# Kernel optimization log

Hardware: AMD Instinct MI355X
Metric: run time of the kernel (lower is better)

## Reference

```python
import jax, jax.numpy as jnp
import numpy as np

NUM_HEAD = 16
D_MODEL = 1024


def setup_inputs() -> dict:
    key = jax.random.key(0)
    ks = jax.random.split(key, 11)
    B, S, D = 2, 2048, D_MODEL
    scale = 1.0 / np.sqrt(D)
    inp = {
        "q": jax.random.normal(ks[0], (B, S, D), dtype=jnp.float32),
        "k": jax.random.normal(ks[1], (B, S, D), dtype=jnp.float32),
        "v": jax.random.normal(ks[2], (B, S, D), dtype=jnp.float32),
        "Wq": jax.random.normal(ks[3], (D, D), dtype=jnp.float32) * scale,
        "bq": jnp.zeros((D,), dtype=jnp.float32),
        "Wk": jax.random.normal(ks[4], (D, D), dtype=jnp.float32) * scale,
        "bk": jnp.zeros((D,), dtype=jnp.float32),
        "Wv": jax.random.normal(ks[5], (D, D), dtype=jnp.float32) * scale,
        "bv": jnp.zeros((D,), dtype=jnp.float32),
        "Wo": jax.random.normal(ks[6], (D, D), dtype=jnp.float32) * scale,
        "bo": jnp.zeros((D,), dtype=jnp.float32),
    }
    return inp


def _split_heads(x, num_head):
    B, S, D = x.shape
    return x.reshape(B, S, num_head, D // num_head).transpose(0, 2, 1, 3)  # [B,H,S,d]


def reference(q, k, v, Wq, bq, Wk, bk, Wv, bv, Wo, bo):
    H = NUM_HEAD
    qp = q @ Wq + bq
    kp = k @ Wk + bk  # computed but UNUSED, matching source bug
    vp = v @ Wv + bv
    # source bug: k := split_heads(v-projection)
    qh = _split_heads(qp, H)          # [B,H,S,d]
    kh = _split_heads(vp, H)          # [B,H,S,d]  (v-projection used as keys)
    vh = _split_heads(vp, H)          # [B,H,S,d]
    d = qh.shape[-1]
    scores = jnp.einsum('bhqd,bhkd->bhqk', qh, kh) / jnp.sqrt(jnp.asarray(d, qh.dtype))
    attn = jax.nn.softmax(scores, axis=-1)
    out = jnp.einsum('bhqk,bhkd->bhqd', attn, vh)  # [B,H,S,d]
    B, _, S, _ = out.shape
    out = out.transpose(0, 2, 1, 3).reshape(B, S, H * d)
    return out @ Wo + bo
```

## Files before the change

kernel.cpp:

```cpp
#include <hip/hip_runtime.h>
#include <hip/hip_bf16.h>

using bfrag  = __attribute__((ext_vector_type(8))) __bf16;
using f32x4  = __attribute__((ext_vector_type(4))) float;
using f32x16 = __attribute__((ext_vector_type(16))) float;
using v4u    = __attribute__((ext_vector_type(4))) unsigned int;
using v2u    = __attribute__((ext_vector_type(2))) unsigned int;

__device__ __forceinline__ ushort f2bf(float f) {
    union { float f; unsigned u; } c; c.f = f;
    return (ushort)((c.u + 0x7fffu + ((c.u >> 16) & 1u)) >> 16);
}

__device__ __forceinline__ float bf2f(ushort u) {
    union { unsigned u; float f; } c; c.u = (unsigned)u << 16; return c.f;
}

__device__ __forceinline__ unsigned pack_bf16x2(float lo, float hi) {
    union { __hip_bfloat162 h; unsigned u; } c;
    c.h = __float22bfloat162_rn(make_float2(lo, hi));
    return c.u;
}

__device__ __forceinline__ void gld_lds16(const ushort* g, ushort* l) {
    __builtin_amdgcn_global_load_lds(
        (const __attribute__((address_space(1))) void*)g,
        (__attribute__((address_space(3))) void*)l, 16, 0, 0);
}

__device__ __forceinline__ f32x16 mfma32(bfrag a, bfrag b, f32x16 c) {
    return __builtin_amdgcn_mfma_f32_32x32x16_bf16(a, b, c, 0, 0, 0);
}


__global__ void cvt_all(const float* __restrict__ s0, ushort* __restrict__ d0,
                        const float* __restrict__ s1, ushort* __restrict__ d1,
                        const float* __restrict__ s2, ushort* __restrict__ d2,
                        const float* __restrict__ q, ushort* __restrict__ qbf,
                        const float* __restrict__ v, ushort* __restrict__ vbf) {
    const int z = blockIdx.z;
    if (z < 3) {
        __shared__ float t[32][33];
        const float* src = z == 0 ? s0 : z == 1 ? s1 : s2;
        ushort* dst = z == 0 ? d0 : z == 1 ? d1 : d2;
        const int tx = threadIdx.x, ty = threadIdx.y;
        const int c0 = blockIdx.x * 32, r0 = blockIdx.y * 32;
        for (int i = ty; i < 32; i += 8) t[i][tx] = src[(size_t)(r0 + i) * 1024 + c0 + tx];
        __syncthreads();
        for (int i = ty; i < 32; i += 8) dst[(size_t)(c0 + i) * 1024 + r0 + tx] = f2bf(t[tx][i]);
    } else {
        const int tid = threadIdx.y * 32 + threadIdx.x;
        int i = ((z - 3) * 1024 + blockIdx.y * 32 + blockIdx.x) * 256 + tid;
        const float* s; ushort* d;
        if (i < 1048576) { s = q; d = qbf; } else { s = v; d = vbf; i -= 1048576; }
        float4 f = ((const float4*)s)[i];
        ((ushort4*)d)[i] = make_ushort4(f2bf(f.x), f2bf(f.y), f2bf(f.z), f2bf(f.w));
    }
}


__global__ __launch_bounds__(256) void vpt_T(const ushort* __restrict__ VPb, ushort* __restrict__ VPT) {
    __shared__ ushort T[64][72];
    const int st = blockIdx.x, bh = blockIdx.y;
    const int b = bh >> 4, h = bh & 15;
    const int tid = threadIdx.x;
#pragma unroll
    for (int i = 0; i < 2; ++i) {
        const int c = tid + i * 256;
        const int row = c >> 3, col8 = (c & 7) * 8;
        v4u d = *(const v4u*)(VPb + (size_t)(b * 2048 + st * 64 + row) * 1024 + h * 64 + col8);
        *(v4u*)&T[row][col8] = d;
    }
    __syncthreads();
    const int d = tid >> 2, sch = tid & 3;
    union { ushort s[16]; v4u v[2]; } tmp;
#pragma unroll
    for (int j = 0; j < 16; ++j) {
        const int js = (j & 3) | ((j >> 1) & 4) | ((j << 1) & 8);
        tmp.s[j] = T[sch * 16 + js][d];
    }
    ushort* dst = VPT + ((size_t)bh * 64 + d) * 2048 + st * 64 + sch * 16;
    *(v4u*)dst = tmp.v[0];
    *(v4u*)(dst + 8) = tmp.v[1];
}


template<bool BF16OUT>
__device__ __forceinline__ void gemm_body(
    const ushort* __restrict__ A, const ushort* __restrict__ Bt,
    const float* __restrict__ bias, void* __restrict__ Cout,
    float scale, int bM, int bN)
{
    __shared__ ushort As[2][64 * 32];
    __shared__ ushort Bs[2][128 * 32];
    const int tid = threadIdx.x;
    const int lane = tid & 63, w = tid >> 6;
    const int l15 = lane & 15, lg = lane >> 4;
    const int wr = w >> 1, wc = w & 1;

    const ushort* Ag = A + (size_t)bM * 64 * 1024;
    const ushort* Bg = Bt + (size_t)bN * 128 * 1024;
    const int ar = tid >> 2;
    const int cc = (tid & 3) * 8;

    auto STAGE = [&](int buf, int kt) {
        const int kk = kt * 32;
        gld_lds16(Ag + (size_t)ar * 1024 + kk + cc, &As[buf][tid * 8]);
#pragma unroll
        for (int i = 0; i < 2; ++i)
            gld_lds16(Bg + (size_t)(ar + i * 64) * 1024 + kk + cc, &Bs[buf][(tid + i * 256) * 8]);
    };

    f32x4 acc[2][4];
#pragma unroll
    for (int m = 0; m < 2; ++m)
#pragma unroll
        for (int n = 0; n < 4; ++n) acc[m][n] = (f32x4){0.f, 0.f, 0.f, 0.f};

    STAGE(0, 0);
    __syncthreads();
    int cur = 0;
    for (int kt = 0; kt < 32; ++kt) {
        if (kt < 31) STAGE(cur ^ 1, kt + 1);
        bfrag aF[2], bF[4];
#pragma unroll
        for (int m = 0; m < 2; ++m) aF[m] = *(const bfrag*)&As[cur][(wr * 32 + m * 16 + l15) * 32 + lg * 8];
#pragma unroll
        for (int n = 0; n < 4; ++n) bF[n] = *(const bfrag*)&Bs[cur][(wc * 64 + n * 16 + l15) * 32 + lg * 8];
        __builtin_amdgcn_s_setprio(1);
#pragma unroll
        for (int m = 0; m < 2; ++m)
#pragma unroll
            for (int n = 0; n < 4; ++n)
                acc[m][n] = __builtin_amdgcn_mfma_f32_16x16x32_bf16(aF[m], bF[n], acc[m][n], 0, 0, 0);
        __builtin_amdgcn_s_setprio(0);
        if (kt < 31) {
            __syncthreads();
            cur ^= 1;
        }
    }

#pragma unroll
    for (int m = 0; m < 2; ++m)
#pragma unroll
        for (int n = 0; n < 4; ++n) {
            const int gcol = bN * 128 + wc * 64 + n * 16 + l15;
            const float bv = bias[gcol];
#pragma unroll
            for (int j = 0; j < 4; ++j) {
                const int grow = bM * 64 + wr * 32 + m * 16 + lg * 4 + j;
                const float val = (acc[m][n][j] + bv) * scale;
                if constexpr (BF16OUT) {
                    ((ushort*)Cout)[(size_t)grow * 1024 + gcol] = f2bf(val);
                } else {
                    ((float*)Cout)[(size_t)grow * 1024 + gcol] = val;
                }
            }
        }
}

__global__ __launch_bounds__(256, 4) void gemm_qv(
    const ushort* __restrict__ Aq, const ushort* __restrict__ Wq, const float* __restrict__ bq, ushort* __restrict__ Cq,
    const ushort* __restrict__ Av, const ushort* __restrict__ Wv, const float* __restrict__ bv, ushort* __restrict__ Cv,
    float qscale)
{
    const int z = blockIdx.z;
    gemm_body<true>(z ? Av : Aq, z ? Wv : Wq, z ? bv : bq, z ? (void*)Cv : (void*)Cq,
                    z ? 1.0f : qscale, blockIdx.y, blockIdx.x);
}

__global__ __launch_bounds__(256, 4) void gemm_o(
    const ushort* __restrict__ A, const ushort* __restrict__ Bt,
    const float* __restrict__ bias, float* __restrict__ Cout)
{
    gemm_body<false>(A, Bt, bias, Cout, 1.0f, blockIdx.y, blockIdx.x);
}


__global__ __launch_bounds__(256, 2) void attn_kernel(
    const ushort* __restrict__ QP, const ushort* __restrict__ VP,
    const ushort* __restrict__ VPT, ushort* __restrict__ Opart, float* __restrict__ Lpart)
{
    __shared__ ushort Ks[2][4096];
    __shared__ ushort Vs[2][4096];
    const int tid = threadIdx.x;
    const int w = tid >> 6, lane = tid & 63;
    const int l31 = lane & 31, hi = lane >> 5;
    const int bh = blockIdx.x, qt = blockIdx.y, half = blockIdx.z;
    const int b = bh >> 4, h = bh & 15;
    const int qrow0 = qt * 256 + w * 64;
    const int k0 = half * 16;

    const int sr = lane >> 3;
    const int sc = ((lane & 7) ^ sr) * 8;
    const ushort* Kg = VP + (size_t)(b * 2048) * 1024 + h * 64 + sc;
    const ushort* Vg = VPT + (size_t)bh * 131072 + sc;

    auto STAGE = [&](int slot, int kt) {
#pragma unroll
        for (int i = 0; i < 2; ++i) {
            const int kb = w * 2 + i;
            const int r = kb * 8 + sr;
            gld_lds16(Kg + (size_t)(kt * 64 + r) * 1024, &Ks[slot][kb * 512]);
            gld_lds16(Vg + (size_t)r * 2048 + kt * 64, &Vs[slot][kb * 512]);
        }
    };

    const ushort* Qp = QP + ((size_t)(b * 2048 + qrow0 + l31)) * 1024 + h * 64 + hi * 8;
    bfrag qA[4], qBt[4];
#pragma unroll
    for (int ds = 0; ds < 4; ++ds) {
        qA[ds]  = *(const bfrag*)(Qp + ds * 16);
        qBt[ds] = *(const bfrag*)(Qp + 32 * 1024 + ds * 16);
    }

    f32x16 OA0, OA1, OB0, OB1;
#pragma unroll
    for (int r = 0; r < 16; ++r) { OA0[r] = 0.f; OA1[r] = 0.f; OB0[r] = 0.f; OB1[r] = 0.f; }
    float lrunA = 0.f, lrunB = 0.f;

    const int swz = (l31 & 7) << 4;
    const int cA = hi * 16;

    STAGE(0, k0);
    __syncthreads();

    auto SOFTMAX = [&](f32x16& S0, f32x16& S1, bfrag (&pB)[4], float& lrun) {
        float p[32];
#pragma unroll
        for (int r = 0; r < 16; ++r) {
            p[r]      = __builtin_amdgcn_exp2f(S0[r]);
            p[16 + r] = __builtin_amdgcn_exp2f(S1[r]);
        }
        float s8[8];
#pragma unroll
        for (int i = 0; i < 8; ++i) s8[i] = (p[i] + p[i + 8]) + (p[i + 16] + p[i + 24]);
        lrun += ((s8[0] + s8[1]) + (s8[2] + s8[3])) + ((s8[4] + s8[5]) + (s8[6] + s8[7]));
#pragma unroll
        for (int c = 0; c < 4; ++c) {
            union { v4u u; bfrag f; } cv;
#pragma unroll
            for (int wd = 0; wd < 4; ++wd)
                cv.u[wd] = pack_bf16x2(p[8 * c + 2 * wd], p[8 * c + 2 * wd + 1]);
            pB[c] = cv.f;
        }
    };

#pragma unroll 1
    for (int t = 0; t < 16; ++t) {
        if (t > 0) __syncthreads();
        if (t + 1 < 16) STAGE((t + 1) & 1, k0 + t + 1);
        const ushort* Kb_ = Ks[t & 1];
        const ushort* Vb_ = Vs[t & 1];

        bfrag k0f[4], k1f[4];
#pragma unroll
        for (int ds = 0; ds < 4; ++ds) {
            k0f[ds] = *(const bfrag*)&Kb_[(l31 * 128 + ((ds * 32 + cA) ^ swz)) >> 1];
            k1f[ds] = *(const bfrag*)&Kb_[((l31 + 32) * 128 + ((ds * 32 + cA) ^ swz)) >> 1];
        }
        f32x16 SA0, SA1, SB0, SB1;
#pragma unroll
        for (int r = 0; r < 16; ++r) { SA0[r] = -16.f; SA1[r] = -16.f; SB0[r] = -16.f; SB1[r] = -16.f; }
        __builtin_amdgcn_s_setprio(1);
#pragma unroll
        for (int ds = 0; ds < 4; ++ds) {
            SA0 = mfma32(k0f[ds], qA[ds], SA0);
            SA1 = mfma32(k1f[ds], qA[ds], SA1);
            SB0 = mfma32(k0f[ds], qBt[ds], SB0);
            SB1 = mfma32(k1f[ds], qBt[ds], SB1);
        }
        __builtin_amdgcn_s_setprio(0);

        bfrag pBA[4], pBB[4];
        SOFTMAX(SA0, SA1, pBA, lrunA);
        SOFTMAX(SB0, SB1, pBB, lrunB);

        bfrag vF0[4], vF1[4];
#pragma unroll
        for (int c = 0; c < 4; ++c) {
            vF0[c] = *(const bfrag*)&Vb_[(l31 * 128 + ((c * 32 + cA) ^ swz)) >> 1];
            vF1[c] = *(const bfrag*)&Vb_[((l31 + 32) * 128 + ((c * 32 + cA) ^ swz)) >> 1];
        }
        __builtin_amdgcn_s_setprio(1);
#pragma unroll
        for (int c = 0; c < 4; ++c) {
            OA0 = mfma32(vF0[c], pBA[c], OA0);
            OA1 = mfma32(vF1[c], pBA[c], OA1);
            OB0 = mfma32(vF0[c], pBB[c], OB0);
            OB1 = mfma32(vF1[c], pBB[c], OB1);
        }
        __builtin_amdgcn_s_setprio(0);
    }

    lrunA += __shfl_xor(lrunA, 32);
    lrunB += __shfl_xor(lrunB, 32);
    ushort* AoA = Opart + (size_t)half * 4194304
                + (size_t)(b * 2048 + qrow0 + l31) * 1024 + h * 64 + hi * 4;
    ushort* AoB = AoA + 32 * 1024;
#pragma unroll
    for (int t = 0; t < 2; ++t) {
#pragma unroll
        for (int g = 0; g < 4; ++g) {
            const float a0 = t ? OA1[4 * g + 0] : OA0[4 * g + 0];
            const float a1 = t ? OA1[4 * g + 1] : OA0[4 * g + 1];
            const float a2 = t ? OA1[4 * g + 2] : OA0[4 * g + 2];
            const float a3 = t ? OA1[4 * g + 3] : OA0[4 * g + 3];
            *(v2u*)(AoA + t * 32 + g * 8) = (v2u){pack_bf16x2(a0, a1), pack_bf16x2(a2, a3)};
            const float b0 = t ? OB1[4 * g + 0] : OB0[4 * g + 0];
            const float b1 = t ? OB1[4 * g + 1] : OB0[4 * g + 1];
            const float b2 = t ? OB1[4 * g + 2] : OB0[4 * g + 2];
            const float b3 = t ? OB1[4 * g + 3] : OB0[4 * g + 3];
            *(v2u*)(AoB + t * 32 + g * 8) = (v2u){pack_bf16x2(b0, b1), pack_bf16x2(b2, b3)};
        }
    }
    if (hi == 0) {
        Lpart[half * 65536 + bh * 2048 + qrow0 + l31] = lrunA;
        Lpart[half * 65536 + bh * 2048 + qrow0 + 32 + l31] = lrunB;
    }
}


__global__ __launch_bounds__(256) void combine_kernel(
    const ushort* __restrict__ Opart, const float* __restrict__ Lpart,
    ushort* __restrict__ AO)
{
    const int t = blockIdx.x * 256 + threadIdx.x;
    const int e0 = t * 8;
    const int grow = e0 >> 10, col = e0 & 1023;
    const int b = grow >> 11, s = grow & 2047, h = col >> 6;
    const int li = (b * 16 + h) * 2048 + s;
    const float l = Lpart[li] + Lpart[65536 + li];
    const float inv = 1.0f / l;
    v4u a = *(const v4u*)(Opart + e0);
    v4u c = *(const v4u*)(Opart + 4194304 + e0);
    v4u o;
#pragma unroll
    for (int wd = 0; wd < 4; ++wd) {
        const float x0 = (bf2f((ushort)(a[wd] & 0xffff)) + bf2f((ushort)(c[wd] & 0xffff))) * inv;
        const float x1 = (bf2f((ushort)(a[wd] >> 16))    + bf2f((ushort)(c[wd] >> 16)))    * inv;
        o[wd] = pack_bf16x2(x0, x1);
    }
    *(v4u*)(AO + e0) = o;
}


extern "C" void kernel_launch(void* const* d_in, const int* in_sizes, int n_in,
                              void* d_out, int out_size, void* d_ws, size_t ws_size,
                              hipStream_t stream) {
    (void)in_sizes; (void)n_in; (void)out_size; (void)ws_size;
    const float* q  = (const float*)d_in[0];
    const float* v  = (const float*)d_in[2];
    const float* Wq = (const float*)d_in[3];
    const float* bq = (const float*)d_in[4];
    const float* Wv = (const float*)d_in[7];
    const float* bv = (const float*)d_in[8];
    const float* Wo = (const float*)d_in[9];
    const float* bo = (const float*)d_in[10];
    float* out = (float*)d_out;
    char* ws = (char*)d_ws;
    const size_t MB = 1ull << 20;
    ushort* qbf = (ushort*)(ws + 0);
    ushort* vbf = (ushort*)(ws + 8 * MB);
    ushort* WqT = (ushort*)(ws + 16 * MB);
    ushort* WvT = (ushort*)(ws + 18 * MB);
    ushort* WoT = (ushort*)(ws + 20 * MB);
    ushort* QPb = (ushort*)(ws + 22 * MB);
    ushort* VPb = (ushort*)(ws + 30 * MB);
    ushort* VPT = (ushort*)(ws + 38 * MB);

    ushort* Opart = (ushort*)(ws + 0);
    float*  Lpart = (float*)(ws + 16 * MB);
    ushort* AO    = QPb;

    cvt_all<<<dim3(32, 32, 11), dim3(32, 8), 0, stream>>>(
        Wq, WqT, Wv, WvT, Wo, WoT, q, qbf, v, vbf);

    const float qscale = 0.125f * 1.44269504088896340736f;
    gemm_qv<<<dim3(8, 64, 2), 256, 0, stream>>>(qbf, WqT, bq, QPb,
                                                vbf, WvT, bv, VPb, qscale);
    vpt_T<<<dim3(32, 32), 256, 0, stream>>>(VPb, VPT);
    attn_kernel<<<dim3(32, 8, 2), 256, 0, stream>>>(QPb, VPb, VPT, Opart, Lpart);
    combine_kernel<<<2048, 256, 0, stream>>>(Opart, Lpart, AO);
    gemm_o<<<dim3(8, 64), 256, 0, stream>>>(AO, WoT, bo, out);
}
```

Baseline: 125.8 us.

## Fuse V transpose into QV GEMM epilogue and split-combine into output GEMM

The QV projection GEMM now stages its bf16 output tile in shared memory and writes the transposed V layout directly, so the separate vpt_T kernel is removed. The output projection GEMM now loads both split-K attention partials and the softmax denominators, combines and normalises them in registers, and writes the A tile to LDS itself, so the combine kernel and its intermediate buffer round trip are removed. This drops two launches and roughly 24MB of global traffic. In exchange, the A operand of gemm_o uses register-staged loads instead of direct-to-LDS copies, and both GEMMs have occupancy hints lowered from 4 to 3.

```diff
diff --git a/kernel.cpp b/kernel.cpp
--- a/kernel.cpp
+++ b/kernel.cpp
@@ -59,44 +59,24 @@
 }
 
 
-__global__ __launch_bounds__(256) void vpt_T(const ushort* __restrict__ VPb, ushort* __restrict__ VPT) {
-    __shared__ ushort T[64][72];
-    const int st = blockIdx.x, bh = blockIdx.y;
-    const int b = bh >> 4, h = bh & 15;
-    const int tid = threadIdx.x;
-#pragma unroll
-    for (int i = 0; i < 2; ++i) {
-        const int c = tid + i * 256;
-        const int row = c >> 3, col8 = (c & 7) * 8;
-        v4u d = *(const v4u*)(VPb + (size_t)(b * 2048 + st * 64 + row) * 1024 + h * 64 + col8);
-        *(v4u*)&T[row][col8] = d;
-    }
-    __syncthreads();
-    const int d = tid >> 2, sch = tid & 3;
-    union { ushort s[16]; v4u v[2]; } tmp;
-#pragma unroll
-    for (int j = 0; j < 16; ++j) {
-        const int js = (j & 3) | ((j >> 1) & 4) | ((j << 1) & 8);
-        tmp.s[j] = T[sch * 16 + js][d];
-    }
-    ushort* dst = VPT + ((size_t)bh * 64 + d) * 2048 + st * 64 + sch * 16;
-    *(v4u*)dst = tmp.v[0];
-    *(v4u*)(dst + 8) = tmp.v[1];
-}
-
-
-template<bool BF16OUT>
-__device__ __forceinline__ void gemm_body(
-    const ushort* __restrict__ A, const ushort* __restrict__ Bt,
-    const float* __restrict__ bias, void* __restrict__ Cout,
-    float scale, int bM, int bN)
+__global__ __launch_bounds__(256, 3) void gemm_qv(
+    const ushort* __restrict__ Aq, const ushort* __restrict__ Wq, const float* __restrict__ bq, ushort* __restrict__ Cq,
+    const ushort* __restrict__ Av, const ushort* __restrict__ Wv, const float* __restrict__ bv, ushort* __restrict__ Cv,
+    ushort* __restrict__ VPT, float qscale)
 {
-    __shared__ ushort As[2][64 * 32];
-    __shared__ ushort Bs[2][128 * 32];
+    __shared__ ushort SM[12288];
+    const int z = blockIdx.z;
+    const ushort* A  = z ? Av : Aq;
+    const ushort* Bt = z ? Wv : Wq;
+    const float* bias = z ? bv : bq;
+    ushort* Cout = z ? Cv : Cq;
+    const float scale = z ? 1.0f : qscale;
+
     const int tid = threadIdx.x;
     const int lane = tid & 63, w = tid >> 6;
     const int l15 = lane & 15, lg = lane >> 4;
     const int wr = w >> 1, wc = w & 1;
+    const int bM = blockIdx.y, bN = blockIdx.x;
 
     const ushort* Ag = A + (size_t)bM * 64 * 1024;
     const ushort* Bg = Bt + (size_t)bN * 128 * 1024;
@@ -105,10 +85,11 @@
 
     auto STAGE = [&](int buf, int kt) {
         const int kk = kt * 32;
-        gld_lds16(Ag + (size_t)ar * 1024 + kk + cc, &As[buf][tid * 8]);
+        gld_lds16(Ag + (size_t)ar * 1024 + kk + cc, &SM[buf * 2048 + tid * 8]);
 #pragma unroll
         for (int i = 0; i < 2; ++i)
-            gld_lds16(Bg + (size_t)(ar + i * 64) * 1024 + kk + cc, &Bs[buf][(tid + i * 256) * 8]);
+            gld_lds16(Bg + (size_t)(ar + i * 64) * 1024 + kk + cc,
+                      &SM[4096 + buf * 4096 + (tid + i * 256) * 8]);
     };
 
     f32x4 acc[2][4];
@@ -124,9 +105,11 @@
         if (kt < 31) STAGE(cur ^ 1, kt + 1);
         bfrag aF[2], bF[4];
 #pragma unroll
-        for (int m = 0; m < 2; ++m) aF[m] = *(const bfrag*)&As[cur][(wr * 32 + m * 16 + l15) * 32 + lg * 8];
-#pragma unroll
-        for (int n = 0; n < 4; ++n) bF[n] = *(const bfrag*)&Bs[cur][(wc * 64 + n * 16 + l15) * 32 + lg * 8];
+        for (int m = 0; m < 2; ++m)
+            aF[m] = *(const bfrag*)&SM[cur * 2048 + (wr * 32 + m * 16 + l15) * 32 + lg * 8];
+#pragma unroll
+        for (int n = 0; n < 4; ++n)
+            bF[n] = *(const bfrag*)&SM[4096 + cur * 4096 + (wc * 64 + n * 16 + l15) * 32 + lg * 8];
         __builtin_amdgcn_s_setprio(1);
 #pragma unroll
         for (int m = 0; m < 2; ++m)
@@ -140,40 +123,140 @@
         }
     }
 
+    __syncthreads();
+#pragma unroll
+    for (int m = 0; m < 2; ++m)
+#pragma unroll
+        for (int n = 0; n < 4; ++n) {
+            const int lcol = wc * 64 + n * 16 + l15;
+            const int gcol = bN * 128 + lcol;
+            const float bv_ = bias[gcol];
+#pragma unroll
+            for (int j = 0; j < 4; ++j) {
+                const int lrow = wr * 32 + m * 16 + lg * 4 + j;
+                const float val = (acc[m][n][j] + bv_) * scale;
+                const ushort hv = f2bf(val);
+                Cout[(size_t)(bM * 64 + lrow) * 1024 + gcol] = hv;
+                if (z) SM[lrow * 129 + lcol] = hv;
+            }
+        }
+
+    if (z) {
+        __syncthreads();
+        const int b_ = (bM * 64) >> 11;
+        const int s0 = (bM * 64) & 2047;
+        const int h0 = bN * 2;
+#pragma unroll
+        for (int i = 0; i < 4; ++i) {
+            const int c2 = i * 256 + tid;
+            const int d128 = c2 >> 3;
+            const int sb = (c2 & 7) * 8;
+            union { ushort s[8]; v4u v; } tmp;
+#pragma unroll
+            for (int jj = 0; jj < 8; ++jj) {
+                const int sl = sb + jj;
+                const int js = (sl & ~15) | (sl & 3) | ((sl >> 1) & 4) | ((sl << 1) & 8);
+                tmp.s[jj] = SM[js * 129 + d128];
+            }
+            ushort* dst = VPT + ((size_t)((b_ * 16 + h0 + (d128 >> 6)) * 64 + (d128 & 63))) * 2048 + s0 + sb;
+            *(v4u*)dst = tmp.v;
+        }
+    }
+}
+
+
+__global__ __launch_bounds__(256, 3) void gemm_o(
+    const ushort* __restrict__ Op0, const ushort* __restrict__ Op1,
+    const float* __restrict__ Lp,
+    const ushort* __restrict__ Bt, const float* __restrict__ bias,
+    float* __restrict__ out)
+{
+    __shared__ ushort As[2][2048];
+    __shared__ ushort Bs[2][4096];
+    const int tid = threadIdx.x;
+    const int lane = tid & 63, w = tid >> 6;
+    const int l15 = lane & 15, lg = lane >> 4;
+    const int wr = w >> 1, wc = w & 1;
+    const int bM = blockIdx.y, bN = blockIdx.x;
+
+    const ushort* Bg = Bt + (size_t)bN * 128 * 1024;
+    const int ar = tid >> 2;
+    const int cc = (tid & 3) * 8;
+    const int grow = bM * 64 + ar;
+    const int b_ = grow >> 11, s_ = grow & 2047;
+
+    v4u aR, cR; float inv;
+    auto LOAD_A = [&](int kt) {
+        const int col = kt * 32 + cc;
+        const int li = (b_ * 16 + (col >> 6)) * 2048 + s_;
+        inv = 1.0f / (Lp[li] + Lp[65536 + li]);
+        aR = *(const v4u*)(Op0 + (size_t)grow * 1024 + col);
+        cR = *(const v4u*)(Op1 + (size_t)grow * 1024 + col);
+    };
+    auto WRITE_A = [&](int buf) {
+        v4u o;
+#pragma unroll
+        for (int wd = 0; wd < 4; ++wd) {
+            const float x0 = (bf2f((ushort)(aR[wd] & 0xffff)) + bf2f((ushort)(cR[wd] & 0xffff))) * inv;
+            const float x1 = (bf2f((ushort)(aR[wd] >> 16))    + bf2f((ushort)(cR[wd] >> 16)))    * inv;
+            o[wd] = pack_bf16x2(x0, x1);
+        }
+        *(v4u*)&As[buf][tid * 8] = o;
+    };
+    auto STAGE_B = [&](int buf, int kt) {
+        const int kk = kt * 32;
+#pragma unroll
+        for (int i = 0; i < 2; ++i)
+            gld_lds16(Bg + (size_t)(ar + i * 64) * 1024 + kk + cc, &Bs[buf][(tid + i * 256) * 8]);
+    };
+
+    f32x4 acc[2][4];
+#pragma unroll
+    for (int m = 0; m < 2; ++m)
+#pragma unroll
+        for (int n = 0; n < 4; ++n) acc[m][n] = (f32x4){0.f, 0.f, 0.f, 0.f};
+
+    LOAD_A(0);
+    STAGE_B(0, 0);
+    WRITE_A(0);
+    __syncthreads();
+    int cur = 0;
+    for (int kt = 0; kt < 32; ++kt) {
+        if (kt < 31) {
+            LOAD_A(kt + 1);
+            STAGE_B(cur ^ 1, kt + 1);
+        }
+        bfrag aF[2], bF[4];
+#pragma unroll
+        for (int m = 0; m < 2; ++m) aF[m] = *(const bfrag*)&As[cur][(wr * 32 + m * 16 + l15) * 32 + lg * 8];
+#pragma unroll
+        for (int n = 0; n < 4; ++n) bF[n] = *(const bfrag*)&Bs[cur][(wc * 64 + n * 16 + l15) * 32 + lg * 8];
+        __builtin_amdgcn_s_setprio(1);
+#pragma unroll
+        for (int m = 0; m < 2; ++m)
+#pragma unroll
+            for (int n = 0; n < 4; ++n)
+                acc[m][n] = __builtin_amdgcn_mfma_f32_16x16x32_bf16(aF[m], bF[n], acc[m][n], 0, 0, 0);
+        __builtin_amdgcn_s_setprio(0);
+        if (kt < 31) {
+            WRITE_A(cur ^ 1);
+            __syncthreads();
+            cur ^= 1;
+        }
+    }
+
 #pragma unroll
     for (int m = 0; m < 2; ++m)
 #pragma unroll
         for (int n = 0; n < 4; ++n) {
             const int gcol = bN * 128 + wc * 64 + n * 16 + l15;
-            const float bv = bias[gcol];
+            const float bv_ = bias[gcol];
 #pragma unroll
             for (int j = 0; j < 4; ++j) {
-                const int grow = bM * 64 + wr * 32 + m * 16 + lg * 4 + j;
-                const float val = (acc[m][n][j] + bv) * scale;
-                if constexpr (BF16OUT) {
-                    ((ushort*)Cout)[(size_t)grow * 1024 + gcol] = f2bf(val);
-                } else {
-                    ((float*)Cout)[(size_t)grow * 1024 + gcol] = val;
-                }
+                const int gr = bM * 64 + wr * 32 + m * 16 + lg * 4 + j;
+                out[(size_t)gr * 1024 + gcol] = acc[m][n][j] + bv_;
             }
         }
-}
-
-__global__ __launch_bounds__(256, 4) void gemm_qv(
-    const ushort* __restrict__ Aq, const ushort* __restrict__ Wq, const float* __restrict__ bq, ushort* __restrict__ Cq,
-    const ushort* __restrict__ Av, const ushort* __restrict__ Wv, const float* __restrict__ bv, ushort* __restrict__ Cv,
-    float qscale)
-{
-    const int z = blockIdx.z;
-    gemm_body<true>(z ? Av : Aq, z ? Wv : Wq, z ? bv : bq, z ? (void*)Cv : (void*)Cq,
-                    z ? 1.0f : qscale, blockIdx.y, blockIdx.x);
-}
-
-__global__ __launch_bounds__(256, 4) void gemm_o(
-    const ushort* __restrict__ A, const ushort* __restrict__ Bt,
-    const float* __restrict__ bias, float* __restrict__ Cout)
-{
-    gemm_body<false>(A, Bt, bias, Cout, 1.0f, blockIdx.y, blockIdx.x);
 }
 
 
@@ -318,30 +401,6 @@
         Lpart[half * 65536 + bh * 2048 + qrow0 + l31] = lrunA;
         Lpart[half * 65536 + bh * 2048 + qrow0 + 32 + l31] = lrunB;
     }
-}
-
-
-__global__ __launch_bounds__(256) void combine_kernel(
-    const ushort* __restrict__ Opart, const float* __restrict__ Lpart,
-    ushort* __restrict__ AO)
-{
-    const int t = blockIdx.x * 256 + threadIdx.x;
-    const int e0 = t * 8;
-    const int grow = e0 >> 10, col = e0 & 1023;
-    const int b = grow >> 11, s = grow & 2047, h = col >> 6;
-    const int li = (b * 16 + h) * 2048 + s;
-    const float l = Lpart[li] + Lpart[65536 + li];
-    const float inv = 1.0f / l;
-    v4u a = *(const v4u*)(Opart + e0);
-    v4u c = *(const v4u*)(Opart + 4194304 + e0);
-    v4u o;
-#pragma unroll
-    for (int wd = 0; wd < 4; ++wd) {
-        const float x0 = (bf2f((ushort)(a[wd] & 0xffff)) + bf2f((ushort)(c[wd] & 0xffff))) * inv;
-        const float x1 = (bf2f((ushort)(a[wd] >> 16))    + bf2f((ushort)(c[wd] >> 16)))    * inv;
-        o[wd] = pack_bf16x2(x0, x1);
-    }
-    *(v4u*)(AO + e0) = o;
 }
 
 
@@ -371,16 +430,13 @@
 
     ushort* Opart = (ushort*)(ws + 0);
     float*  Lpart = (float*)(ws + 16 * MB);
-    ushort* AO    = QPb;
 
     cvt_all<<<dim3(32, 32, 11), dim3(32, 8), 0, stream>>>(
         Wq, WqT, Wv, WvT, Wo, WoT, q, qbf, v, vbf);
 
     const float qscale = 0.125f * 1.44269504088896340736f;
     gemm_qv<<<dim3(8, 64, 2), 256, 0, stream>>>(qbf, WqT, bq, QPb,
-                                                vbf, WvT, bv, VPb, qscale);
-    vpt_T<<<dim3(32, 32), 256, 0, stream>>>(VPb, VPT);
+                                                vbf, WvT, bv, VPb, VPT, qscale);
     attn_kernel<<<dim3(32, 8, 2), 256, 0, stream>>>(QPb, VPb, VPT, Opart, Lpart);
-    combine_kernel<<<2048, 256, 0, stream>>>(Opart, Lpart, AO);
-    gemm_o<<<dim3(8, 64), 256, 0, stream>>>(AO, WoT, bo, out);
-}
+    gemm_o<<<dim3(8, 64), 256, 0, stream>>>(Opart, Opart + 4194304, Lpart, WoT, bo, out);
+}
```

Result: no change. 124.1 us (median of 3 runs) (-1.3%).
